# Kernel optimization log

Hardware: AMD Instinct MI355X
Metric: run time of the kernel (lower is better)

## Reference

```python
import jax, jax.numpy as jnp
import numpy as np

N = 100000
E = 800000
DROPOUT_P = 0.5


def setup_inputs() -> dict:
    key = jax.random.key(0)
    ks = jax.random.split(key, 5)
    x = jax.random.normal(ks[0], (N, 128), dtype=jnp.float32)
    edge_index = jax.random.randint(ks[1], (2, E), 0, N, dtype=jnp.int32)
    # Glorot-ish init for the two GCNConv weight matrices
    W1 = jax.random.normal(ks[2], (128, 512), dtype=jnp.float32) * (1.0 / np.sqrt(128))
    b1 = jnp.zeros((512,), dtype=jnp.float32)
    W2 = jax.random.normal(ks[3], (512, 40), dtype=jnp.float32) * (1.0 / np.sqrt(512))
    b2 = jnp.zeros((40,), dtype=jnp.float32)
    return {"x": x, "edge_index": edge_index, "W1": W1, "b1": b1, "W2": W2, "b2": b2}


def _gcn_norm(edge_index, num_nodes):
    # PyG GCNConv: add self-loops, symmetric normalization D^{-1/2} (A+I) D^{-1/2}
    loop = jnp.arange(num_nodes, dtype=edge_index.dtype)
    src = jnp.concatenate([edge_index[0], loop])
    dst = jnp.concatenate([edge_index[1], loop])
    deg = jax.ops.segment_sum(jnp.ones_like(dst, dtype=jnp.float32), dst,
                              num_segments=num_nodes)
    deg_inv_sqrt = jax.lax.rsqrt(deg)  # deg >= 1 thanks to self-loops
    norm = deg_inv_sqrt[src] * deg_inv_sqrt[dst]  # [E+N]
    return src, dst, norm


def _gcn_conv(x, src, dst, norm, W, b, num_nodes):
    h = x @ W                                   # [N, out] dense GEMM first (out <= in here)
    msg = h[src] * norm[:, None]                # gather + scale: [E+N, out]
    out = jax.ops.segment_sum(msg, dst, num_segments=num_nodes)  # scatter-add
    return out + b


def reference(x, edge_index, W1, b1, W2, b2):
    src, dst, norm = _gcn_norm(edge_index, N)
    h = _gcn_conv(x, src, dst, norm, W1, b1, N)
    h = jax.nn.relu(h)
    # dropout p=0.5, training=True, deterministic mask
    keep = jax.random.bernoulli(jax.random.key(42), 1.0 - DROPOUT_P, h.shape)
    h = jnp.where(keep, h / (1.0 - DROPOUT_P), 0.0)
    hidden = h
    out = _gcn_conv(h, src, dst, norm, W2, b2, N)
    return out, hidden
```

## Files before the change

### kernel.cpp

```cpp
#include <hip/hip_runtime.h>
#include <hip/hip_bf16.h>
#include <stdint.h>

typedef __attribute__((ext_vector_type(8))) __bf16 bf16x8;
typedef __attribute__((ext_vector_type(8))) unsigned short ushort8;
typedef __attribute__((ext_vector_type(4))) float f32x4;
typedef __attribute__((ext_vector_type(4))) unsigned int u32x4;

#define N_NODES 100000
#define N_EDGES 800000
#define FIN 128
#define FH 512
#define FO 40
#define NCHUNK 391
#define TWBLKS 352

#define O_DINV   0ull
#define O_CNT    400000ull
#define O_ROWPTR 800000ull
#define O_CUR    1200016ull
#define O_SRC    1600016ull
#define O_DSRC   4800016ull
#define O_W1T    8000016ull
#define O_W2T    8131088ull
#define O_AXG    8180240ull
#define O_H2     59380240ull
#define O_PART   75380240ull

__device__ __forceinline__ unsigned short f2bf(float f) {
  unsigned u = __float_as_uint(f);
  u += 0x7fffu + ((u >> 16) & 1u);
  return (unsigned short)(u >> 16);
}

__device__ __forceinline__ bf16x8 pack8t(u32x4 a, u32x4 b) {
  u32x4 w;
  w.x = __builtin_amdgcn_perm(a.y, a.x, 0x07060302u);
  w.y = __builtin_amdgcn_perm(a.w, a.z, 0x07060302u);
  w.z = __builtin_amdgcn_perm(b.y, b.x, 0x07060302u);
  w.w = __builtin_amdgcn_perm(b.w, b.z, 0x07060302u);
  return __builtin_bit_cast(bf16x8, w);
}


__global__ __launch_bounds__(256) void k_count(const int* __restrict__ dst,
                                               int* __restrict__ cnt) {
  int e = blockIdx.x * 256 + threadIdx.x;
  if (e < N_EDGES) atomicAdd(&cnt[__builtin_nontemporal_load(&dst[e])], 1);
}


__global__ __launch_bounds__(256) void k_scan1tw(const int* __restrict__ cnt,
                                                 int* __restrict__ rowptr,
                                                 int* __restrict__ partials,
                                                 float* __restrict__ dinv,
                                                 const float* __restrict__ w1,
                                                 const float* __restrict__ w2,
                                                 unsigned short* __restrict__ w1t,
                                                 unsigned short* __restrict__ w2t) {
  int b = blockIdx.x;
  if (b >= NCHUNK) {
    int t = (b - NCHUNK) * 256 + threadIdx.x;
    if (t < FIN * FH) {
      int c = t >> 7, k = t & 127;
      w1t[c * 128 + k] = f2bf(w1[k * FH + c]);
    } else {
      int u = t - FIN * FH;
      int c = u >> 9, k = u & 511;
      w2t[c * FH + k] = (c < FO) ? f2bf(w2[k * FO + c]) : (unsigned short)0;
    }
    return;
  }
  int t = threadIdx.x, g = b * 256 + t;
  int v = (g < N_NODES) ? cnt[g] : 0;
  if (g < N_NODES) dinv[g] = __frsqrt_rn((float)(v + 1));
  int lane = t & 63, w = t >> 6;
  int sc = v;
#pragma unroll
  for (int off = 1; off < 64; off <<= 1) {
    int u = __shfl_up(sc, off);
    if (lane >= off) sc += u;
  }
  __shared__ int wsum[4];
  if (lane == 63) wsum[w] = sc;
  __syncthreads();
  int add = 0;
  for (int j = 0; j < w; j++) add += wsum[j];
  int incl = sc + add;
  if (g < N_NODES) rowptr[g] = incl - v;
  if (t == 255) partials[b] = incl;
}


__global__ __launch_bounds__(256) void k_scan3(int* __restrict__ rowptr,
                                               const int* __restrict__ partials,
                                               int* __restrict__ cur) {
  __shared__ int sbase;
  int t = threadIdx.x;
  int chunk = blockIdx.x;
  if (t < 64) {
    int s = 0;
    for (int j = t; j < chunk; j += 64) s += partials[j];
#pragma unroll
    for (int off = 32; off; off >>= 1) s += __shfl_down(s, off);
    if (t == 0) sbase = s;
  }
  __syncthreads();
  int base = sbase;
  int g = chunk * 256 + t;
  if (g < N_NODES) {
    int v = rowptr[g] + base;
    rowptr[g] = v;
    cur[g] = v;
  } else if (g == N_NODES) {
    rowptr[N_NODES] = N_EDGES;
  }
}

__global__ __launch_bounds__(256) void k_scatter(const int* __restrict__ src,
                                                 const int* __restrict__ dst,
                                                 const float* __restrict__ dinv,
                                                 int* __restrict__ cur,
                                                 int* __restrict__ src_sorted,
                                                 float* __restrict__ dinv_src) {
  int e = blockIdx.x * 256 + threadIdx.x;
  if (e < N_EDGES) {
    int s = __builtin_nontemporal_load(&src[e]);
    int d = __builtin_nontemporal_load(&dst[e]);
    int pos = atomicAdd(&cur[d], 1);
    src_sorted[pos] = s;
    dinv_src[pos] = dinv[s];
  }
}


__device__ __forceinline__ unsigned tf_bits(unsigned x0, unsigned x1) {
  const unsigned K0 = 0u, K1 = 42u, K2 = 0x1BD11BDAu ^ 42u;
  x0 += K0; x1 += K1;
#define RND(r) { x0 += x1; x1 = (x1 << (r)) | (x1 >> (32 - (r))); x1 ^= x0; }
  RND(13) RND(15) RND(26) RND(6)
  x0 += K1; x1 += K2 + 1u;
  RND(17) RND(29) RND(16) RND(24)
  x0 += K2; x1 += K0 + 2u;
  RND(13) RND(15) RND(26) RND(6)
  x0 += K0; x1 += K1 + 3u;
  RND(17) RND(29) RND(16) RND(24)
  x0 += K1; x1 += K2 + 4u;
  RND(13) RND(15) RND(26) RND(6)
  x0 += K2; x1 += K0 + 5u;
#undef RND
  return x0 ^ x1;
}


__global__ __launch_bounds__(256) void k_aggx(const float* __restrict__ x,
                                              const int* __restrict__ rowptr,
                                              const int* __restrict__ src_sorted,
                                              const float* __restrict__ dinv_src,
                                              const float* __restrict__ dinv,
                                              float* __restrict__ axg,
                                              unsigned char* __restrict__ mask8) {
  int i = blockIdx.x * 4 + (threadIdx.x >> 6);
  int lane = threadIdx.x & 63;
  int rs = rowptr[i], re = rowptr[i + 1];
  float di = dinv[i];
  int c = lane << 1;

  {
    unsigned fb = (unsigned)i * FH + ((unsigned)lane << 3);
    unsigned mb = 0;
#pragma unroll
    for (int q = 0; q < 8; q++)
      mb |= ((~tf_bits(0u, fb + q)) >> 31) << q;
    mask8[((size_t)i << 6) | lane] = (unsigned char)mb;
  }

  float a0 = 0.0f, a1 = 0.0f;

  for (int base = rs; base < re; base += 64) {
    int n = re - base; if (n > 64) n = 64;
    int myi = 0; float myw = 0.0f;
    if (lane < n) {
      myi = src_sorted[base + lane];
      myw = dinv_src[base + lane];
    }
    int j = 0;
    for (; j + 4 <= n; j += 4) {
      int s0 = __shfl(myi, j),     s1 = __shfl(myi, j + 1);
      int s2 = __shfl(myi, j + 2), s3 = __shfl(myi, j + 3);
      float w0 = __shfl(myw, j),      w1_ = __shfl(myw, j + 1);
      float w2_ = __shfl(myw, j + 2), w3_ = __shfl(myw, j + 3);
      float2 v0 = *(const float2*)(x + (((size_t)s0 << 7) | c));
      float2 v1 = *(const float2*)(x + (((size_t)s1 << 7) | c));
      float2 v2 = *(const float2*)(x + (((size_t)s2 << 7) | c));
      float2 v3 = *(const float2*)(x + (((size_t)s3 << 7) | c));
      a0 += w0 * v0.x + w1_ * v1.x + w2_ * v2.x + w3_ * v3.x;
      a1 += w0 * v0.y + w1_ * v1.y + w2_ * v2.y + w3_ * v3.y;
    }
    for (; j < n; j++) {
      int s0 = __shfl(myi, j);
      float w0 = __shfl(myw, j);
      float2 v0 = *(const float2*)(x + (((size_t)s0 << 7) | c));
      a0 += w0 * v0.x; a1 += w0 * v0.y;
    }
  }
  {
    float2 vs = *(const float2*)(x + (((size_t)i << 7) | c));
    a0 += di * vs.x; a1 += di * vs.y;
  }
  float2 o; o.x = a0 * di; o.y = a1 * di;
  *(float2*)(axg + (((size_t)i << 7) | c)) = o;
}


__global__ __launch_bounds__(256) void k_gemm1f(const float* __restrict__ axg,
                                                const unsigned short* __restrict__ w1t,
                                                const float* __restrict__ b1,
                                                const unsigned char* __restrict__ mask8,
                                                float* __restrict__ hidden) {
  int w = threadIdx.x >> 6;
  int lane = threadIdx.x & 63;
  int m = lane & 15, kg = lane >> 4;
  int r0 = blockIdx.x * 32;
  int cw = w * 128;
  f32x4 acc[2][8];
#pragma unroll
  for (int a = 0; a < 2; a++)
#pragma unroll
    for (int t = 0; t < 8; t++)
#pragma unroll
      for (int r = 0; r < 4; r++) acc[a][t][r] = 0.0f;

  const float* xa0 = axg + (size_t)(r0 + m) * FIN + kg * 8;
  const float* xa1 = xa0 + 16 * FIN;
#pragma unroll
  for (int kc = 0; kc < 4; kc++) {
    int kb = kc * 32;
    u32x4 a0l = *(const u32x4*)(xa0 + kb);
    u32x4 a0h = *(const u32x4*)(xa0 + kb + 4);
    u32x4 a1l = *(const u32x4*)(xa1 + kb);
    u32x4 a1h = *(const u32x4*)(xa1 + kb + 4);
    bf16x8 a0 = pack8t(a0l, a0h);
    bf16x8 a1 = pack8t(a1l, a1h);
#pragma unroll
    for (int t = 0; t < 8; t++) {
      const unsigned short* bp = w1t + (size_t)(cw + t * 16 + m) * FIN + kb + kg * 8;
      bf16x8 b = __builtin_bit_cast(bf16x8, *(const ushort8*)bp);
      acc[0][t] = __builtin_amdgcn_mfma_f32_16x16x32_bf16(a0, b, acc[0][t], 0, 0, 0);
      acc[1][t] = __builtin_amdgcn_mfma_f32_16x16x32_bf16(a1, b, acc[1][t], 0, 0, 0);
    }
  }

  float bcol[8];
#pragma unroll
  for (int t = 0; t < 8; t++) bcol[t] = b1[cw + t * 16 + m];

  u32x4 mv[2][4];
#pragma unroll
  for (int rt = 0; rt < 2; rt++)
#pragma unroll
    for (int r = 0; r < 4; r++) {
      int row = r0 + rt * 16 + kg * 4 + r;
      mv[rt][r] = *(const u32x4*)(mask8 + (size_t)row * 64 + w * 16);
    }

#pragma unroll
  for (int rt = 0; rt < 2; rt++)
#pragma unroll
    for (int t = 0; t < 8; t++)
#pragma unroll
      for (int r = 0; r < 4; r++) {
        int row = r0 + rt * 16 + kg * 4 + r;
        int col = cw + t * 16 + m;
        unsigned flat = (unsigned)row * FH + (unsigned)col;
        float v = fmaxf(acc[rt][t][r] + bcol[t], 0.0f);
        unsigned keep = (mv[rt][r][t >> 1] >> ((t & 1) * 16 + m)) & 1u;
        hidden[flat] = keep ? v * 2.0f : 0.0f;
      }
}


__global__ __launch_bounds__(256) void k_gemm2(const float* __restrict__ hidden,
                                               const unsigned short* __restrict__ w2t,
                                               float* __restrict__ h2) {
  int wid = blockIdx.x * 4 + (threadIdx.x >> 6);
  if (wid >= N_NODES / 16) return;
  int lane = threadIdx.x & 63;
  int m = lane & 15, kg = lane >> 4;
  int r0 = wid * 16;
  f32x4 acc[3];
#pragma unroll
  for (int t = 0; t < 3; t++)
#pragma unroll
    for (int r = 0; r < 4; r++) acc[t][r] = 0.0f;

  const float* ap = hidden + (size_t)(r0 + m) * FH + kg * 8;
#pragma unroll 8
  for (int kc = 0; kc < 16; kc++) {
    int kb = kc * 32;
    u32x4 al = __builtin_nontemporal_load((const u32x4*)(ap + kb));
    u32x4 ah = __builtin_nontemporal_load((const u32x4*)(ap + kb + 4));
    bf16x8 a = pack8t(al, ah);
#pragma unroll
    for (int t = 0; t < 3; t++) {
      bf16x8 b = __builtin_bit_cast(bf16x8,
          *(const ushort8*)(w2t + (size_t)(t * 16 + m) * FH + kb + kg * 8));
      acc[t] = __builtin_amdgcn_mfma_f32_16x16x32_bf16(a, b, acc[t], 0, 0, 0);
    }
  }
#pragma unroll
  for (int t = 0; t < 3; t++)
#pragma unroll
    for (int r = 0; r < 4; r++) {
      int row = r0 + kg * 4 + r;
      int col = t * 16 + m;
      if (col < FO) h2[(size_t)row * FO + col] = acc[t][r];
    }
}


__global__ __launch_bounds__(256) void k_agg2(const float* __restrict__ h2,
                                              const int* __restrict__ rowptr,
                                              const int* __restrict__ src_sorted,
                                              const float* __restrict__ dinv_src,
                                              const float* __restrict__ dinv,
                                              const float* __restrict__ b2,
                                              float* __restrict__ out) {
  int i = blockIdx.x * 4 + (threadIdx.x >> 6);
  int lane = threadIdx.x & 63;
  int rs = rowptr[i], re = rowptr[i + 1];
  float di = dinv[i];
  float acc = 0.0f;

  for (int base = rs; base < re; base += 64) {
    int n = re - base; if (n > 64) n = 64;
    int myi = 0; float myw = 0.0f;
    if (lane < n) {
      myi = __builtin_nontemporal_load(&src_sorted[base + lane]);
      myw = __builtin_nontemporal_load(&dinv_src[base + lane]);
    }
    for (int j = 0; j < n; j++) {
      int s = __shfl(myi, j);
      float wgt = __shfl(myw, j);
      if (lane < FO) acc += wgt * h2[(size_t)s * FO + lane];
    }
  }
  if (lane < FO) {
    acc += di * h2[(size_t)i * FO + lane];
    out[(size_t)i * FO + lane] = acc * di + b2[lane];
  }
}


extern "C" void kernel_launch(void* const* d_in, const int* in_sizes, int n_in,
                              void* d_out, int out_size, void* d_ws, size_t ws_size,
                              hipStream_t stream) {
  const float* x  = (const float*)d_in[0];
  const int* ei   = (const int*)d_in[1];
  const float* w1 = (const float*)d_in[2];
  const float* b1 = (const float*)d_in[3];
  const float* w2 = (const float*)d_in[4];
  const float* b2 = (const float*)d_in[5];

  char* ws = (char*)d_ws;
  float* dinv            = (float*)(ws + O_DINV);
  int* cnt               = (int*)(ws + O_CNT);
  int* rowptr            = (int*)(ws + O_ROWPTR);
  int* cur               = (int*)(ws + O_CUR);
  int* src_sorted        = (int*)(ws + O_SRC);
  float* dinv_src        = (float*)(ws + O_DSRC);
  unsigned short* w1t    = (unsigned short*)(ws + O_W1T);
  unsigned short* w2t    = (unsigned short*)(ws + O_W2T);
  float* axg             = (float*)(ws + O_AXG);
  float* h2              = (float*)(ws + O_H2);
  unsigned char* mask8   = (unsigned char*)(ws + O_H2);
  int* partials          = (int*)(ws + O_PART);

  float* outp   = (float*)d_out;
  float* hidden = outp + (size_t)N_NODES * FO;

  const int* srcA = ei;
  const int* dstA = ei + N_EDGES;

  hipMemsetAsync(cnt, 0, N_NODES * sizeof(int), stream);
  k_count<<<(N_EDGES + 255) / 256, 256, 0, stream>>>(dstA, cnt);
  k_scan1tw<<<NCHUNK + TWBLKS, 256, 0, stream>>>(cnt, rowptr, partials, dinv,
                                                 w1, w2, w1t, w2t);
  k_scan3<<<NCHUNK, 256, 0, stream>>>(rowptr, partials, cur);
  k_scatter<<<(N_EDGES + 255) / 256, 256, 0, stream>>>(srcA, dstA, dinv, cur,
                                                       src_sorted, dinv_src);
  k_aggx<<<N_NODES / 4, 256, 0, stream>>>(x, rowptr, src_sorted, dinv_src, dinv,
                                          axg, mask8);
  k_gemm1f<<<N_NODES / 32, 256, 0, stream>>>(axg, w1t, b1, mask8, hidden);
  k_gemm2<<<(N_NODES / 16 + 3) / 4, 256, 0, stream>>>(hidden, w2t, h2);
  k_agg2<<<N_NODES / 4, 256, 0, stream>>>(h2, rowptr, src_sorted, dinv_src, dinv,
                                          b2, outp);
}
```

Baseline: 662.2 us.

## Fuse second GEMM into first GEMM epilogue via LDS-staged bf16 hidden tile

```diff
diff --git a/kernel.cpp b/kernel.cpp
--- a/kernel.cpp
+++ b/kernel.cpp
@@ -26,6 +26,7 @@
 #define O_AXG    8180240ull
 #define O_H2     59380240ull
 #define O_PART   75380240ull
+#define O_MASK   75400000ull
 
 __device__ __forceinline__ unsigned short f2bf(float f) {
   unsigned u = __float_as_uint(f);
@@ -213,11 +214,14 @@
 }
 
 
-__global__ __launch_bounds__(256) void k_gemm1f(const float* __restrict__ axg,
+__global__ __launch_bounds__(256) void k_gemm12(const float* __restrict__ axg,
                                                 const unsigned short* __restrict__ w1t,
                                                 const float* __restrict__ b1,
                                                 const unsigned char* __restrict__ mask8,
-                                                float* __restrict__ hidden) {
+                                                const unsigned short* __restrict__ w2t,
+                                                float* __restrict__ hidden,
+                                                float* __restrict__ h2) {
+  __shared__ __align__(16) char smem[32768];
   int w = threadIdx.x >> 6;
   int lane = threadIdx.x & 63;
   int m = lane & 15, kg = lane >> 4;
@@ -270,52 +274,61 @@
     for (int t = 0; t < 8; t++)
 #pragma unroll
       for (int r = 0; r < 4; r++) {
-        int row = r0 + rt * 16 + kg * 4 + r;
+        int rowl = rt * 16 + kg * 4 + r;
         int col = cw + t * 16 + m;
-        unsigned flat = (unsigned)row * FH + (unsigned)col;
+        unsigned flat = (unsigned)(r0 + rowl) * FH + (unsigned)col;
         float v = fmaxf(acc[rt][t][r] + bcol[t], 0.0f);
         unsigned keep = (mv[rt][r][t >> 1] >> ((t & 1) * 16 + m)) & 1u;
-        hidden[flat] = keep ? v * 2.0f : 0.0f;
+        float hv = keep ? v * 2.0f : 0.0f;
+        hidden[flat] = hv;
+        unsigned short hb = (unsigned short)(__float_as_uint(hv) >> 16);
+        *(unsigned short*)(smem + rowl * 1024 + ((col * 2) ^ ((rowl & 15) << 4))) = hb;
       }
-}
-
-
-__global__ __launch_bounds__(256) void k_gemm2(const float* __restrict__ hidden,
-                                               const unsigned short* __restrict__ w2t,
-                                               float* __restrict__ h2) {
-  int wid = blockIdx.x * 4 + (threadIdx.x >> 6);
-  if (wid >= N_NODES / 16) return;
-  int lane = threadIdx.x & 63;
-  int m = lane & 15, kg = lane >> 4;
-  int r0 = wid * 16;
-  f32x4 acc[3];
-#pragma unroll
-  for (int t = 0; t < 3; t++)
-#pragma unroll
-    for (int r = 0; r < 4; r++) acc[t][r] = 0.0f;
-
-  const float* ap = hidden + (size_t)(r0 + m) * FH + kg * 8;
-#pragma unroll 8
-  for (int kc = 0; kc < 16; kc++) {
-    int kb = kc * 32;
-    u32x4 al = __builtin_nontemporal_load((const u32x4*)(ap + kb));
-    u32x4 ah = __builtin_nontemporal_load((const u32x4*)(ap + kb + 4));
-    bf16x8 a = pack8t(al, ah);
-#pragma unroll
-    for (int t = 0; t < 3; t++) {
-      bf16x8 b = __builtin_bit_cast(bf16x8,
-          *(const ushort8*)(w2t + (size_t)(t * 16 + m) * FH + kb + kg * 8));
-      acc[t] = __builtin_amdgcn_mfma_f32_16x16x32_bf16(a, b, acc[t], 0, 0, 0);
-    }
-  }
-#pragma unroll
-  for (int t = 0; t < 3; t++)
-#pragma unroll
-    for (int r = 0; r < 4; r++) {
-      int row = r0 + kg * 4 + r;
-      int col = t * 16 + m;
-      if (col < FO) h2[(size_t)row * FO + col] = acc[t][r];
-    }
+  __syncthreads();
+
+  f32x4 acc2[2][3];
+#pragma unroll
+  for (int rt = 0; rt < 2; rt++)
+#pragma unroll
+    for (int t = 0; t < 3; t++)
+#pragma unroll
+      for (int r = 0; r < 4; r++) acc2[rt][t][r] = 0.0f;
+
+#pragma unroll
+  for (int kc = 0; kc < 4; kc++) {
+    int colk = cw + kc * 32 + kg * 8;
+#pragma unroll
+    for (int rt = 0; rt < 2; rt++) {
+      int rowl = rt * 16 + m;
+      bf16x8 a = *(const bf16x8*)(smem + rowl * 1024 + ((colk * 2) ^ ((rowl & 15) << 4)));
+#pragma unroll
+      for (int t = 0; t < 3; t++) {
+        bf16x8 b = __builtin_bit_cast(bf16x8,
+            *(const ushort8*)(w2t + (size_t)(t * 16 + m) * FH + colk));
+        acc2[rt][t] = __builtin_amdgcn_mfma_f32_16x16x32_bf16(a, b, acc2[rt][t], 0, 0, 0);
+      }
+    }
+  }
+  __syncthreads();
+
+  float* part = (float*)smem;
+#pragma unroll
+  for (int rt = 0; rt < 2; rt++)
+#pragma unroll
+    for (int t = 0; t < 3; t++)
+#pragma unroll
+      for (int r = 0; r < 4; r++) {
+        int rowl = rt * 16 + kg * 4 + r;
+        int coln = t * 16 + m;
+        part[w * 1536 + rowl * 48 + coln] = acc2[rt][t][r];
+      }
+  __syncthreads();
+
+  for (int idx = threadIdx.x; idx < 1536; idx += 256) {
+    int rowl = idx / 48, coln = idx - rowl * 48;
+    float s = part[idx] + part[1536 + idx] + part[3072 + idx] + part[4608 + idx];
+    if (coln < FO) h2[(size_t)(r0 + rowl) * FO + coln] = s;
+  }
 }
 
 
@@ -373,7 +386,7 @@
   unsigned short* w2t    = (unsigned short*)(ws + O_W2T);
   float* axg             = (float*)(ws + O_AXG);
   float* h2              = (float*)(ws + O_H2);
-  unsigned char* mask8   = (unsigned char*)(ws + O_H2);
+  unsigned char* mask8   = (unsigned char*)(ws + O_MASK);
   int* partials          = (int*)(ws + O_PART);
 
   float* outp   = (float*)d_out;
@@ -391,8 +404,7 @@
                                                        src_sorted, dinv_src);
   k_aggx<<<N_NODES / 4, 256, 0, stream>>>(x, rowptr, src_sorted, dinv_src, dinv,
                                           axg, mask8);
-  k_gemm1f<<<N_NODES / 32, 256, 0, stream>>>(axg, w1t, b1, mask8, hidden);
-  k_gemm2<<<(N_NODES / 16 + 3) / 4, 256, 0, stream>>>(hidden, w2t, h2);
+  k_gemm12<<<N_NODES / 32, 256, 0, stream>>>(axg, w1t, b1, mask8, w2t, hidden, h2);
   k_agg2<<<N_NODES / 4, 256, 0, stream>>>(h2, rowptr, src_sorted, dinv_src, dinv,
                                           b2, outp);
 }
```

Result: faster. 623.4 us (-5.9%).
